# Kernel tuning notes

Measured on AMD Instinct MI355X. Metric: run time of the kernel, lower is better.

## Reference

```python
import jax, jax.numpy as jnp
import numpy as np

TOP_K = 8
NORM_TOPK_PROB = False


def setup_inputs() -> dict:
    key = jax.random.key(0)
    k1, k2 = jax.random.split(key)
    hidden_states = jax.random.normal(k1, (4, 8192, 2048), dtype=jnp.float32)
    # gate weight: [n_experts=64, hidden_dim=2048], like nn.Linear weight
    weight = jax.random.normal(k2, (64, 2048), dtype=jnp.float32) * 0.02
    return {"hidden_states": hidden_states, "weight": weight}


def reference(hidden_states, weight):
    hidden_dim = weight.shape[1]
    x = hidden_states.reshape(-1, hidden_dim)            # [N, D]
    router_logits = jnp.einsum('nd,ed->ne', x, weight)   # [N, E] F.linear
    # softmax in float32 (dtype=torch.float), returned as the "logits"
    router_probs = jax.nn.softmax(router_logits.astype(jnp.float32), axis=-1)
    router_top_value, router_indices = jax.lax.top_k(router_probs, TOP_K)
    if NORM_TOPK_PROB:
        router_top_value = router_top_value / jnp.sum(router_top_value, axis=-1, keepdims=True)
    router_top_value = router_top_value.astype(router_probs.dtype)
    return (router_probs, router_top_value, router_indices)
```

## Files before the change

kernel.cpp:

```cpp
#include <hip/hip_runtime.h>
#include <math.h>


constexpr int HD = 2048, NE = 64, TOPK = 8;
constexpr float XSC = 4096.f;
constexpr float WSC = 8192.f;
constexpr float DESCALE = 1.0f / (XSC * WSC);

typedef _Float16 f16x8 __attribute__((ext_vector_type(8)));
typedef float f32x4 __attribute__((ext_vector_type(4)));

__global__ __launch_bounds__(256)
void wprep_k(const float* __restrict__ W, char* __restrict__ WP) {
  const int n = blockIdx.x, t = threadIdx.x;
  const float* src = W + n * HD + t * 8;
  f16x8 hi, lo;
#pragma unroll
  for (int j = 0; j < 8; ++j) {
    float a = src[j] * WSC;
    _Float16 h = (_Float16)a;
    hi[j] = h;
    lo[j] = (_Float16)(a - (float)h);
  }
  char* dst = WP + n * 8192 + t * 32;
  *(f16x8*)dst = hi;
  *(f16x8*)(dst + 16) = lo;
}

__global__ __launch_bounds__(256, 4)
void router_k(const float* __restrict__ X, const char* __restrict__ WP,
              float* __restrict__ probs, float* __restrict__ topv,
              float* __restrict__ topi) {
  __shared__ float part[4][16][68];

  const int tid = threadIdx.x, wv = tid >> 6, lane = tid & 63;
  const int m = lane & 15, q = lane >> 4;
  const int rowbase = blockIdx.x * 32;
  const int rg = wv >> 1, h = wv & 1;

  const float* xp = X + (size_t)(rowbase + rg * 16 + m) * HD + h * 1024 + q * 8;
  const char* wp0 = WP + m * 8192 + h * 4096 + q * 32;

  f32x4 acc_hh[4], acc_cr[4];
#pragma unroll
  for (int nt = 0; nt < 4; ++nt) {
    acc_hh[nt] = {0.f, 0.f, 0.f, 0.f};
    acc_cr[nt] = {0.f, 0.f, 0.f, 0.f};
  }

  f32x4 xaA, xbA, xaB, xbB, xaC, xbC;
  f16x8 wf[8];

#define LOADX(XA, XB, kk) { XA = *(const f32x4*)(xp + (kk) * 32);          \
                            XB = *(const f32x4*)(xp + (kk) * 32 + 4); }
#define LOADW(kk) { _Pragma("unroll")                                      \
    for (int nt = 0; nt < 4; ++nt) {                                       \
      wf[2*nt]   = *(const f16x8*)(wp0 + nt * 131072 + (kk) * 128);        \
      wf[2*nt+1] = *(const f16x8*)(wp0 + nt * 131072 + (kk) * 128 + 16); } }
#define STEP(XA, XB) {                                                     \
    f16x8 ah, al;                                                          \
    _Pragma("unroll") for (int j = 0; j < 4; ++j) {                        \
      float a = XA[j] * XSC; _Float16 ha = (_Float16)a;                    \
      ah[j] = ha; al[j] = (_Float16)(a - (float)ha);                       \
      float b = XB[j] * XSC; _Float16 hb = (_Float16)b;                    \
      ah[j+4] = hb; al[j+4] = (_Float16)(b - (float)hb); }                 \
    _Pragma("unroll") for (int nt = 0; nt < 4; ++nt) {                     \
      acc_hh[nt] = __builtin_amdgcn_mfma_f32_16x16x32_f16(ah, wf[2*nt],   acc_hh[nt], 0, 0, 0); \
      acc_cr[nt] = __builtin_amdgcn_mfma_f32_16x16x32_f16(ah, wf[2*nt+1], acc_cr[nt], 0, 0, 0); \
      acc_cr[nt] = __builtin_amdgcn_mfma_f32_16x16x32_f16(al, wf[2*nt],   acc_cr[nt], 0, 0, 0); } }

  LOADX(xaA, xbA, 0);
  LOADX(xaB, xbB, 1);
  for (int k3 = 0; k3 < 10; ++k3) {
    const int k0 = 3 * k3;
    LOADX(xaC, xbC, k0 + 2);  LOADW(k0);      STEP(xaA, xbA);
    LOADX(xaA, xbA, k0 + 3);  LOADW(k0 + 1);  STEP(xaB, xbB);
    LOADX(xaB, xbB, k0 + 4);  LOADW(k0 + 2);  STEP(xaC, xbC);
  }
  LOADW(30);  STEP(xaA, xbA);
  LOADW(31);  STEP(xaB, xbB);

#undef LOADX
#undef LOADW
#undef STEP

#pragma unroll
  for (int nt = 0; nt < 4; ++nt)
#pragma unroll
    for (int r = 0; r < 4; ++r)
      part[wv][4 * q + r][nt * 16 + m] = (acc_hh[nt][r] + acc_cr[nt][r]) * DESCALE;
  __syncthreads();

  for (int rr = 0; rr < 8; ++rr) {
    const int rb = wv * 8 + rr;
    const int pi = (rb >> 4) * 2, ri = rb & 15;
    const float lg = part[pi][ri][lane] + part[pi + 1][ri][lane];

    float mx = lg;
#pragma unroll
    for (int off = 32; off; off >>= 1)
      mx = fmaxf(mx, __shfl_xor(mx, off, 64));

    const float ex = expf(lg - mx);
    float sm = ex;
#pragma unroll
    for (int off = 32; off; off >>= 1)
      sm += __shfl_xor(sm, off, 64);

    const float p = ex * (1.0f / sm);
    probs[(size_t)(rowbase + rb) * NE + lane] = p;

    int rank = 0;
#pragma unroll
    for (int j = 0; j < NE; ++j) {
      const float pj = __shfl(p, j, 64);
      rank += (pj > p) || (pj == p && j < lane);
    }
    if (rank < TOPK) {
      topv[(size_t)(rowbase + rb) * TOPK + rank] = p;
      topi[(size_t)(rowbase + rb) * TOPK + rank] = (float)lane;
    }
  }
}

extern "C" void kernel_launch(void* const* d_in, const int* in_sizes, int n_in,
                              void* d_out, int out_size, void* d_ws, size_t ws_size,
                              hipStream_t stream) {
  const float* X = (const float*)d_in[0];
  const float* W = (const float*)d_in[1];
  const int n = in_sizes[0] / HD;

  float* probs = (float*)d_out;
  float* topv  = probs + (size_t)n * NE;
  float* topi  = topv + (size_t)n * TOPK;
  char* WP = (char*)d_ws;

  hipLaunchKernelGGL(wprep_k, dim3(NE), dim3(256), 0, stream, W, WP);
  hipLaunchKernelGGL(router_k, dim3(n / 32), dim3(256), 0, stream,
                     X, WP, probs, topv, topi);
}
```

Baseline: 457.8 us.

## Double rows per wave and repack weights into lane-contiguous MFMA fragments

Each wave now computes 32 rows instead of 16, so each weight fragment loaded from global memory feeds two row groups of MFMAs. The packed weight layout is rearranged so that per-k-step fragments are contiguous by lane and coalesced, with hi/lo split into separate 1KB planes. The main loop now double-buffers the weight fragments. Register pressure roughly doubles, so launch bounds drop to 2 blocks per SIMD and the grid is halved.

```diff
diff --git a/kernel.cpp b/kernel.cpp
--- a/kernel.cpp
+++ b/kernel.cpp
@@ -12,73 +12,93 @@
 
 __global__ __launch_bounds__(256)
 void wprep_k(const float* __restrict__ W, char* __restrict__ WP) {
-  const int n = blockIdx.x, t = threadIdx.x;
-  const float* src = W + n * HD + t * 8;
+  const int b = blockIdx.x;
+  const int h = b >> 5, kk = b & 31;
+  const int t = threadIdx.x;
+  const int nt = t >> 6, q = (t >> 4) & 3, m = t & 15;
+  const float* src = W + (size_t)(nt * 16 + m) * HD + h * 1024 + kk * 32 + q * 8;
   f16x8 hi, lo;
 #pragma unroll
   for (int j = 0; j < 8; ++j) {
     float a = src[j] * WSC;
-    _Float16 h = (_Float16)a;
-    hi[j] = h;
-    lo[j] = (_Float16)(a - (float)h);
+    _Float16 ha = (_Float16)a;
+    hi[j] = ha;
+    lo[j] = (_Float16)(a - (float)ha);
   }
-  char* dst = WP + n * 8192 + t * 32;
+  char* dst = WP + ((size_t)b * 8 + nt * 2) * 1024 + (q * 16 + m) * 16;
   *(f16x8*)dst = hi;
-  *(f16x8*)(dst + 16) = lo;
+  *(f16x8*)(dst + 1024) = lo;
 }
 
-__global__ __launch_bounds__(256, 4)
+__global__ __launch_bounds__(256, 2)
 void router_k(const float* __restrict__ X, const char* __restrict__ WP,
               float* __restrict__ probs, float* __restrict__ topv,
               float* __restrict__ topi) {
-  __shared__ float part[4][16][68];
+  __shared__ float part[4][32][68];
 
   const int tid = threadIdx.x, wv = tid >> 6, lane = tid & 63;
   const int m = lane & 15, q = lane >> 4;
-  const int rowbase = blockIdx.x * 32;
+  const int rowbase = blockIdx.x * 64;
   const int rg = wv >> 1, h = wv & 1;
 
-  const float* xp = X + (size_t)(rowbase + rg * 16 + m) * HD + h * 1024 + q * 8;
-  const char* wp0 = WP + m * 8192 + h * 4096 + q * 32;
+  const float* xq0 = X + (size_t)(rowbase + rg * 32 + m) * HD + h * 1024 + q * 8;
+  const float* xq1 = xq0 + 16 * HD;
+  const char* wq = WP + (size_t)h * 262144 + lane * 16;
 
-  f32x4 acc_hh[4], acc_cr[4];
+  f32x4 acc_hh0[4], acc_cr0[4], acc_hh1[4], acc_cr1[4];
 #pragma unroll
   for (int nt = 0; nt < 4; ++nt) {
-    acc_hh[nt] = {0.f, 0.f, 0.f, 0.f};
-    acc_cr[nt] = {0.f, 0.f, 0.f, 0.f};
+    acc_hh0[nt] = {0.f, 0.f, 0.f, 0.f}; acc_cr0[nt] = {0.f, 0.f, 0.f, 0.f};
+    acc_hh1[nt] = {0.f, 0.f, 0.f, 0.f}; acc_cr1[nt] = {0.f, 0.f, 0.f, 0.f};
   }
 
-  f32x4 xaA, xbA, xaB, xbB, xaC, xbC;
-  f16x8 wf[8];
+  f32x4 x0aA, x0bA, x1aA, x1bA, x0aB, x0bB, x1aB, x1bB;
+  f16x8 w0[8], w1[8];
 
-#define LOADX(XA, XB, kk) { XA = *(const f32x4*)(xp + (kk) * 32);          \
-                            XB = *(const f32x4*)(xp + (kk) * 32 + 4); }
-#define LOADW(kk) { _Pragma("unroll")                                      \
-    for (int nt = 0; nt < 4; ++nt) {                                       \
-      wf[2*nt]   = *(const f16x8*)(wp0 + nt * 131072 + (kk) * 128);        \
-      wf[2*nt+1] = *(const f16x8*)(wp0 + nt * 131072 + (kk) * 128 + 16); } }
-#define STEP(XA, XB) {                                                     \
-    f16x8 ah, al;                                                          \
-    _Pragma("unroll") for (int j = 0; j < 4; ++j) {                        \
-      float a = XA[j] * XSC; _Float16 ha = (_Float16)a;                    \
-      ah[j] = ha; al[j] = (_Float16)(a - (float)ha);                       \
-      float b = XB[j] * XSC; _Float16 hb = (_Float16)b;                    \
-      ah[j+4] = hb; al[j+4] = (_Float16)(b - (float)hb); }                 \
-    _Pragma("unroll") for (int nt = 0; nt < 4; ++nt) {                     \
-      acc_hh[nt] = __builtin_amdgcn_mfma_f32_16x16x32_f16(ah, wf[2*nt],   acc_hh[nt], 0, 0, 0); \
-      acc_cr[nt] = __builtin_amdgcn_mfma_f32_16x16x32_f16(ah, wf[2*nt+1], acc_cr[nt], 0, 0, 0); \
-      acc_cr[nt] = __builtin_amdgcn_mfma_f32_16x16x32_f16(al, wf[2*nt],   acc_cr[nt], 0, 0, 0); } }
+#define LOADX(S, OFF) {                                             \
+    x0a##S = *(const f32x4*)((const char*)xq0 + (OFF));             \
+    x0b##S = *(const f32x4*)((const char*)xq0 + (OFF) + 16);        \
+    x1a##S = *(const f32x4*)((const char*)xq1 + (OFF));             \
+    x1b##S = *(const f32x4*)((const char*)xq1 + (OFF) + 16); }
+#define LOADW(WF, OFF) { _Pragma("unroll")                          \
+    for (int nt = 0; nt < 4; ++nt) {                                \
+      WF[2*nt]   = *(const f16x8*)(wq + (OFF) + nt * 2048);         \
+      WF[2*nt+1] = *(const f16x8*)(wq + (OFF) + nt * 2048 + 1024); } }
+#define STEP(S, WF) {                                               \
+    f16x8 ah0, al0, ah1, al1;                                       \
+    _Pragma("unroll") for (int j = 0; j < 4; ++j) {                 \
+      float a0 = x0a##S[j] * XSC; _Float16 h0 = (_Float16)a0;       \
+      ah0[j] = h0; al0[j] = (_Float16)(a0 - (float)h0);             \
+      float b0 = x0b##S[j] * XSC; _Float16 g0 = (_Float16)b0;       \
+      ah0[j+4] = g0; al0[j+4] = (_Float16)(b0 - (float)g0);         \
+      float a1 = x1a##S[j] * XSC; _Float16 h1 = (_Float16)a1;       \
+      ah1[j] = h1; al1[j] = (_Float16)(a1 - (float)h1);             \
+      float b1 = x1b##S[j] * XSC; _Float16 g1 = (_Float16)b1;       \
+      ah1[j+4] = g1; al1[j+4] = (_Float16)(b1 - (float)g1); }       \
+    _Pragma("unroll") for (int nt = 0; nt < 4; ++nt) {              \
+      acc_hh0[nt] = __builtin_amdgcn_mfma_f32_16x16x32_f16(ah0, WF[2*nt],   acc_hh0[nt], 0, 0, 0); \
+      acc_cr0[nt] = __builtin_amdgcn_mfma_f32_16x16x32_f16(ah0, WF[2*nt+1], acc_cr0[nt], 0, 0, 0); \
+      acc_cr0[nt] = __builtin_amdgcn_mfma_f32_16x16x32_f16(al0, WF[2*nt],   acc_cr0[nt], 0, 0, 0); \
+      acc_hh1[nt] = __builtin_amdgcn_mfma_f32_16x16x32_f16(ah1, WF[2*nt],   acc_hh1[nt], 0, 0, 0); \
+      acc_cr1[nt] = __builtin_amdgcn_mfma_f32_16x16x32_f16(ah1, WF[2*nt+1], acc_cr1[nt], 0, 0, 0); \
+      acc_cr1[nt] = __builtin_amdgcn_mfma_f32_16x16x32_f16(al1, WF[2*nt],   acc_cr1[nt], 0, 0, 0); } }
 
-  LOADX(xaA, xbA, 0);
-  LOADX(xaB, xbB, 1);
-  for (int k3 = 0; k3 < 10; ++k3) {
-    const int k0 = 3 * k3;
-    LOADX(xaC, xbC, k0 + 2);  LOADW(k0);      STEP(xaA, xbA);
-    LOADX(xaA, xbA, k0 + 3);  LOADW(k0 + 1);  STEP(xaB, xbB);
-    LOADX(xaB, xbB, k0 + 4);  LOADW(k0 + 2);  STEP(xaC, xbC);
+  LOADX(A, 0);
+  LOADX(B, 128);
+  LOADW(w0, 0);
+
+  for (int i = 0; i < 15; ++i) {
+    LOADW(w1, 8192);
+    STEP(A, w0);
+    LOADX(A, 256);
+    LOADW(w0, 16384);
+    STEP(B, w1);
+    LOADX(B, 384);
+    xq0 += 64; xq1 += 64; wq += 16384;
   }
-  LOADW(30);  STEP(xaA, xbA);
-  LOADW(31);  STEP(xaB, xbB);
+  LOADW(w1, 8192);
+  STEP(A, w0);
+  STEP(B, w1);
 
 #undef LOADX
 #undef LOADW
@@ -87,14 +107,18 @@
 #pragma unroll
   for (int nt = 0; nt < 4; ++nt)
 #pragma unroll
-    for (int r = 0; r < 4; ++r)
-      part[wv][4 * q + r][nt * 16 + m] = (acc_hh[nt][r] + acc_cr[nt][r]) * DESCALE;
+    for (int r = 0; r < 4; ++r) {
+      part[wv][4 * q + r][nt * 16 + m] =
+          (acc_hh0[nt][r] + acc_cr0[nt][r]) * DESCALE;
+      part[wv][16 + 4 * q + r][nt * 16 + m] =
+          (acc_hh1[nt][r] + acc_cr1[nt][r]) * DESCALE;
+    }
   __syncthreads();
 
-  for (int rr = 0; rr < 8; ++rr) {
-    const int rb = wv * 8 + rr;
-    const int pi = (rb >> 4) * 2, ri = rb & 15;
-    const float lg = part[pi][ri][lane] + part[pi + 1][ri][lane];
+  for (int rr = 0; rr < 16; ++rr) {
+    const int rb = wv * 16 + rr;
+    const int rgx = rb >> 5, r = rb & 31;
+    const float lg = part[2 * rgx][r][lane] + part[2 * rgx + 1][r][lane];
 
     float mx = lg;
 #pragma unroll
@@ -135,7 +159,7 @@
   float* topi  = topv + (size_t)n * TOPK;
   char* WP = (char*)d_ws;
 
-  hipLaunchKernelGGL(wprep_k, dim3(NE), dim3(256), 0, stream, W, WP);
-  hipLaunchKernelGGL(router_k, dim3(n / 32), dim3(256), 0, stream,
+  hipLaunchKernelGGL(wprep_k, dim3(64), dim3(256), 0, stream, W, WP);
+  hipLaunchKernelGGL(router_k, dim3(n / 64), dim3(256), 0, stream,
                      X, WP, probs, topv, topi);
 }
```

After: 428.6 us. 6.4% less time.
